# Performance work log

Measured on AMD Instinct MI355X. Metric: run time of the kernel, lower is better.

## Reference

```python
import jax, jax.numpy as jnp
import numpy as np

N = 50000
DEG = 16
E = N * DEG
IN_F, HID, OUT_F = 512, 128, 64
SLOPE = 0.2


def setup_inputs() -> dict:
    key = jax.random.key(0)
    ks = jax.random.split(key, 10)
    row_ptr = jnp.arange(N + 1, dtype=jnp.int64) * DEG          # uniform-degree CSR
    col_idx = jax.random.randint(ks[0], (E,), 0, N, dtype=jnp.int64)
    x = jax.random.normal(ks[1], (N, IN_F), dtype=jnp.float32)
    s1 = 1.0 / np.sqrt(IN_F)
    s2 = 1.0 / np.sqrt(HID)
    return {
        "row_ptr": row_ptr,
        "col_idx": col_idx,
        "input_feature": x,
        "W1": jax.random.normal(ks[2], (IN_F, HID), dtype=jnp.float32) * s1,
        "attn_l1": jax.random.normal(ks[3], (HID,), dtype=jnp.float32) * s2,
        "attn_r1": jax.random.normal(ks[4], (HID,), dtype=jnp.float32) * s2,
        "bias1": jnp.zeros((HID,), dtype=jnp.float32),
        "W2": jax.random.normal(ks[5], (HID, OUT_F), dtype=jnp.float32) * s2,
        "attn_l2": jax.random.normal(ks[6], (OUT_F,), dtype=jnp.float32) * 0.125,
        "attn_r2": jax.random.normal(ks[7], (OUT_F,), dtype=jnp.float32) * 0.125,
        "bias2": jnp.zeros((OUT_F,), dtype=jnp.float32),
    }


def gat_layer(row_ptr, col_idx, x, W, attn_l, attn_r, bias):
    n = row_ptr.shape[0] - 1
    e = col_idx.shape[0]
    h = x @ W                                   # [N, F] dense GEMM
    el = h @ attn_l                             # [N] dst attention term
    er = h @ attn_r                             # [N] src attention term
    # edge -> destination row via CSR row_ptr
    dst = jnp.searchsorted(row_ptr, jnp.arange(e, dtype=row_ptr.dtype), side="right") - 1
    src = col_idx
    score = jax.nn.leaky_relu(el[dst] + er[src], negative_slope=SLOPE)  # [E]
    # neighborhood softmax over edges sharing a destination
    smax = jax.ops.segment_max(score, dst, num_segments=n)
    ex = jnp.exp(score - smax[dst])
    ssum = jax.ops.segment_sum(ex, dst, num_segments=n)
    alpha = ex / ssum[dst]                      # [E]
    # weighted gather-scatter aggregation
    out = jax.ops.segment_sum(alpha[:, None] * h[src], dst, num_segments=n)
    return out + bias


def reference(row_ptr, col_idx, input_feature, W1, attn_l1, attn_r1, bias1,
              W2, attn_l2, attn_r2, bias2):
    x = gat_layer(row_ptr, col_idx, input_feature, W1, attn_l1, attn_r1, bias1)
    x = gat_layer(row_ptr, col_idx, x, W2, attn_l2, attn_r2, bias2)
    return x
```

## Files before the change

kernel.cpp:

```cpp
#include <hip/hip_runtime.h>
#include <hip/hip_bf16.h>

#define Nn 50000
#define DEG 16
#define IN_F 512
#define HID 128
#define OUT_F 64
#define SLOPE 0.2f

typedef __attribute__((ext_vector_type(8))) short bf16x8;
typedef __attribute__((ext_vector_type(4))) float f32x4;
typedef __attribute__((ext_vector_type(4))) unsigned int u32x4;

__device__ __forceinline__ unsigned short f2bf(float f) {
    return __builtin_bit_cast(unsigned short, __float2bfloat16(f));
}
__device__ __forceinline__ float bf2f(unsigned short u) {
    return __bfloat162float(__builtin_bit_cast(__hip_bfloat16, u));
}

__global__ void __launch_bounds__(256) prep_kernel(
        const float* __restrict__ W1, const float* __restrict__ W2,
        const float* __restrict__ al1, const float* __restrict__ ar1,
        const float* __restrict__ b1, const int* __restrict__ row_ptr,
        unsigned short* __restrict__ w12t, float* __restrict__ uv,
        float* __restrict__ c2v, int* __restrict__ flag64) {
    const int tid = threadIdx.x;
    const int lane = tid & 63;
    const int w = tid >> 6;
    const int k = blockIdx.x * 4 + w;
    if (blockIdx.x == 0 && tid == 0) {
        *flag64 = (row_ptr[1] == DEG) ? 0 : 1;
    }
    const float* w1row = W1 + (size_t)k * HID;

    float acc = 0.f;
    #pragma unroll 8
    for (int j = 0; j < HID; ++j)
        acc += w1row[j] * W2[j * OUT_F + lane];
    w12t[(size_t)lane * IN_F + k] = f2bf(acc);

    float pu = w1row[lane] * al1[lane] + w1row[lane + 64] * al1[lane + 64];
    float pv = w1row[lane] * ar1[lane] + w1row[lane + 64] * ar1[lane + 64];
    #pragma unroll
    for (int m = 1; m < 64; m <<= 1) {
        pu += __shfl_xor(pu, m);
        pv += __shfl_xor(pv, m);
    }
    if (lane == 0) { uv[k] = pu; uv[IN_F + k] = pv; }

    if (blockIdx.x == 0 && w == 0) {
        float cacc = 0.f;
        #pragma unroll 8
        for (int j = 0; j < HID; ++j) cacc += b1[j] * W2[j * OUT_F + lane];
        c2v[lane] = cacc;
    }
}

template<int K>
__global__ void __launch_bounds__(256, 6) gemm1_splitk(
        const float* __restrict__ Af, const unsigned short* __restrict__ w12t,
        const float* __restrict__ uv,
        unsigned short* __restrict__ G, float* __restrict__ el,
        float* __restrict__ er, int M) {
    constexpr int KW = K / 4;
    constexpr int RS = 20;
    __shared__ float red[4][64][RS];
    __shared__ float redl[4][16];
    __shared__ float redr[4][16];

    const int tid  = threadIdx.x;
    const int lane = tid & 63;
    const int w    = tid >> 6;
    const int ln   = lane & 15, q = lane >> 4;
    const int mb   = blockIdx.x * 16;

    const float* a0p = Af + (size_t)(mb + ln) * K + w * KW + q * 8;
    const float* up  = uv + w * KW + q * 8;
    const float* vp  = uv + K + w * KW + q * 8;

    f32x4 acc[4] = {};
    float sl = 0.f, sr = 0.f;

    f32x4 cur0 = *(const f32x4*)(a0p);
    f32x4 cur1 = *(const f32x4*)(a0p + 4);
    #pragma unroll
    for (int ks = 0; ks < 4; ++ks) {
        f32x4 nxt0, nxt1;
        if (ks < 3) {
            nxt0 = *(const f32x4*)(a0p + (ks + 1) * 32);
            nxt1 = *(const f32x4*)(a0p + (ks + 1) * 32 + 4);
        }
        f32x4 u0 = *(const f32x4*)(up + ks * 32);
        f32x4 u1 = *(const f32x4*)(up + ks * 32 + 4);
        f32x4 v0 = *(const f32x4*)(vp + ks * 32);
        f32x4 v1 = *(const f32x4*)(vp + ks * 32 + 4);
        bf16x8 af;
        #pragma unroll
        for (int jj = 0; jj < 4; ++jj) {
            af[jj]     = (short)f2bf(cur0[jj]);
            af[jj + 4] = (short)f2bf(cur1[jj]);
            sl += cur0[jj] * u0[jj] + cur1[jj] * u1[jj];
            sr += cur0[jj] * v0[jj] + cur1[jj] * v1[jj];
        }
        #pragma unroll
        for (int nt = 0; nt < 4; ++nt) {
            bf16x8 bfr = *(const bf16x8*)
                &w12t[(size_t)(nt * 16 + ln) * K + w * KW + ks * 32 + q * 8];
            acc[nt] = __builtin_amdgcn_mfma_f32_16x16x32_bf16(af, bfr, acc[nt], 0, 0, 0);
        }
        if (ks < 3) { cur0 = nxt0; cur1 = nxt1; }
    }

    #pragma unroll
    for (int nt = 0; nt < 4; ++nt)
        *(f32x4*)&red[w][nt * 16 + ln][q * 4] = acc[nt];

    sl += __shfl_xor(sl, 16); sl += __shfl_xor(sl, 32);
    sr += __shfl_xor(sr, 16); sr += __shfl_xor(sr, 32);
    if (q == 0) { redl[w][ln] = sl; redr[w][ln] = sr; }
    __syncthreads();

    const int c  = tid & 63;
    const int r0 = (tid >> 6) * 4;
    f32x4 s = *(const f32x4*)&red[0][c][r0];
    #pragma unroll
    for (int ww = 1; ww < 4; ++ww) {
        f32x4 p = *(const f32x4*)&red[ww][c][r0];
        s += p;
    }
    #pragma unroll
    for (int j = 0; j < 4; ++j)
        G[(size_t)(mb + r0 + j) * OUT_F + c] = f2bf(s[j]);

    if (tid < 16) {
        el[mb + tid] = redl[0][tid] + redl[1][tid] + redl[2][tid] + redl[3][tid];
        er[mb + tid] = redr[0][tid] + redr[1][tid] + redr[2][tid] + redr[3][tid];
    }
}

template<int MODE>
__global__ void __launch_bounds__(256) agg_k(
        const int* __restrict__ col, const int* __restrict__ flag64,
        const float* __restrict__ el, const float* __restrict__ er,
        const unsigned short* __restrict__ Hs, const float* __restrict__ addv,
        const float* __restrict__ alv, const float* __restrict__ arv,
        unsigned short* __restrict__ Ho, float* __restrict__ elo,
        float* __restrict__ ero, float* __restrict__ Fo) {
    const int tid  = threadIdx.x;
    const int lane = tid & 63;
    const int w    = tid >> 6;
    const int ln   = lane & 15, q = lane >> 4;
    const int g16  = w * 4 + q;
    const int nA   = blockIdx.x * 32 + g16 * 2;
    const int nB   = nA + 1;
    const int nAc  = nA < Nn ? nA : Nn - 1;
    const int nBc  = nB < Nn ? nB : Nn - 1;
    const int use64 = *flag64;

    int eA = nAc * DEG + ln, eB = nBc * DEG + ln;
    int srcA = use64 ? (int)((const long long*)col)[eA] : col[eA];
    int srcB = use64 ? (int)((const long long*)col)[eB] : col[eB];
    float scA = el[nAc] + er[srcA];
    float scB = el[nBc] + er[srcB];
    scA = scA >= 0.f ? scA : SLOPE * scA;
    scB = scB >= 0.f ? scB : SLOPE * scB;
    float mxA = scA, mxB = scB;
    #pragma unroll
    for (int m = 1; m < 16; m <<= 1) {
        mxA = fmaxf(mxA, __shfl_xor(mxA, m, 16));
        mxB = fmaxf(mxB, __shfl_xor(mxB, m, 16));
    }
    float exA = __expf(scA - mxA), exB = __expf(scB - mxB);
    float smA = exA, smB = exB;
    #pragma unroll
    for (int m = 1; m < 16; m <<= 1) {
        smA += __shfl_xor(smA, m, 16);
        smB += __shfl_xor(smB, m, 16);
    }
    float alA = exA / smA, alB = exB / smB;

    const int half = ln >> 3, cc = ln & 7;
    float aA[8] = {}, aB[8] = {};
    #pragma unroll
    for (int jj = 0; jj < DEG; jj += 2) {
        int   sjA = __shfl(srcA, jj + half, 16);
        float ajA = __shfl(alA,  jj + half, 16);
        int   sjB = __shfl(srcB, jj + half, 16);
        float ajB = __shfl(alB,  jj + half, 16);
        bf16x8 hA = *(const bf16x8*)&Hs[(size_t)sjA * OUT_F + cc * 8];
        bf16x8 hB = *(const bf16x8*)&Hs[(size_t)sjB * OUT_F + cc * 8];
        #pragma unroll
        for (int c = 0; c < 8; ++c) {
            aA[c] += ajA * bf2f((unsigned short)hA[c]);
            aB[c] += ajB * bf2f((unsigned short)hB[c]);
        }
    }
    #pragma unroll
    for (int c = 0; c < 8; ++c) {
        aA[c] += __shfl_xor(aA[c], 8, 16);
        aB[c] += __shfl_xor(aB[c], 8, 16);
        float ad = addv[cc * 8 + c];
        aA[c] += ad;
        aB[c] += ad;
    }

    if (MODE == 0) {
        float plA = 0.f, prA = 0.f, plB = 0.f, prB = 0.f;
        #pragma unroll
        for (int c = 0; c < 8; ++c) {
            float av = alv[cc * 8 + c], bv = arv[cc * 8 + c];
            plA += aA[c] * av;  prA += aA[c] * bv;
            plB += aB[c] * av;  prB += aB[c] * bv;
        }
        #pragma unroll
        for (int m = 1; m < 8; m <<= 1) {
            plA += __shfl_xor(plA, m, 16);  prA += __shfl_xor(prA, m, 16);
            plB += __shfl_xor(plB, m, 16);  prB += __shfl_xor(prB, m, 16);
        }
        if (ln == 0) {
            if (nA < Nn) { elo[nA] = plA; ero[nA] = prA; }
            if (nB < Nn) { elo[nB] = plB; ero[nB] = prB; }
        }
        if (half == 0) {
            unsigned int pkA[4], pkB[4];
            #pragma unroll
            for (int c = 0; c < 4; ++c) {
                pkA[c] = (unsigned int)f2bf(aA[2 * c]) |
                         ((unsigned int)f2bf(aA[2 * c + 1]) << 16);
                pkB[c] = (unsigned int)f2bf(aB[2 * c]) |
                         ((unsigned int)f2bf(aB[2 * c + 1]) << 16);
            }
            if (nA < Nn) *(u32x4*)&Ho[(size_t)nA * OUT_F + cc * 8] = *(u32x4*)pkA;
            if (nB < Nn) *(u32x4*)&Ho[(size_t)nB * OUT_F + cc * 8] = *(u32x4*)pkB;
        }
    } else {
        if (half == 0) {
            f32x4 oA0, oA1, oB0, oB1;
            #pragma unroll
            for (int c = 0; c < 4; ++c) {
                oA0[c] = aA[c]; oA1[c] = aA[c + 4];
                oB0[c] = aB[c]; oB1[c] = aB[c + 4];
            }
            if (nA < Nn) {
                *(f32x4*)&Fo[(size_t)nA * OUT_F + cc * 8]     = oA0;
                *(f32x4*)&Fo[(size_t)nA * OUT_F + cc * 8 + 4] = oA1;
            }
            if (nB < Nn) {
                *(f32x4*)&Fo[(size_t)nB * OUT_F + cc * 8]     = oB0;
                *(f32x4*)&Fo[(size_t)nB * OUT_F + cc * 8 + 4] = oB1;
            }
        }
    }
}

extern "C" void kernel_launch(void* const* d_in, const int* in_sizes, int n_in,
                              void* d_out, int out_size, void* d_ws, size_t ws_size,
                              hipStream_t stream) {
    const int*   row_ptr = (const int*)d_in[0];
    const int*   col_idx = (const int*)d_in[1];
    const float* x   = (const float*)d_in[2];
    const float* W1  = (const float*)d_in[3];
    const float* al1 = (const float*)d_in[4];
    const float* ar1 = (const float*)d_in[5];
    const float* b1  = (const float*)d_in[6];
    const float* W2  = (const float*)d_in[7];
    const float* al2 = (const float*)d_in[8];
    const float* ar2 = (const float*)d_in[9];
    const float* b2  = (const float*)d_in[10];
    float* out = (float*)d_out;

    float* ws = (float*)d_ws;
    unsigned short* g   = (unsigned short*)ws;
    unsigned short* h2b = (unsigned short*)(ws + 1600000);
    float* el1 = ws + 3200000;
    float* er1 = ws + 3250000;
    float* el2 = ws + 3300000;
    float* er2 = ws + 3350000;
    unsigned short* w12t = (unsigned short*)(ws + 3400000);
    float* uv  = ws + 3420000;
    float* c2v = ws + 3421024;
    int* flag64 = (int*)(ws + 3421100);

    prep_kernel<<<128, 256, 0, stream>>>(
        W1, W2, al1, ar1, b1, row_ptr, w12t, uv, c2v, flag64);

    gemm1_splitk<IN_F><<<Nn / 16, 256, 0, stream>>>(
        x, w12t, uv, g, el1, er1, Nn);

    agg_k<0><<<(Nn + 31) / 32, 256, 0, stream>>>(
        col_idx, flag64, el1, er1, g, c2v, al2, ar2, h2b, el2, er2, nullptr);

    agg_k<1><<<(Nn + 31) / 32, 256, 0, stream>>>(
        col_idx, flag64, el2, er2, h2b, b2, nullptr, nullptr,
        nullptr, nullptr, nullptr, out);
}
```

Measured before the change: 235.3 us.

## Replace split-K GEMM with 64-row tiled GEMM using async global-to-LDS loads

The first GEMM moves from a 16-row split-K layout, which needed a cross-wave LDS reduction, to 64-row tiles. Each wave now owns 16 rows over the full K, stepping through 128-wide chunks staged in LDS with global_load_lds async copies. The fused W1·W2 weight is stored pre-chunked with an XOR swizzle so its LDS reads avoid bank conflicts, and each block reuses it across 64 rows instead of 16. The cost is 48KB of LDS per block, which limits occupancy, and loads are not double-buffered, so each chunk waits at a barrier with no overlap.

Result: faster. 223.3 us (-5.1%).

```diff
diff --git a/kernel.cpp b/kernel.cpp
--- a/kernel.cpp
+++ b/kernel.cpp
@@ -18,12 +18,17 @@
 __device__ __forceinline__ float bf2f(unsigned short u) {
     return __bfloat162float(__builtin_bit_cast(__hip_bfloat16, u));
 }
+__device__ __forceinline__ void async_copy16(const void* g, void* l) {
+    __builtin_amdgcn_global_load_lds(
+        (const __attribute__((address_space(1))) unsigned int*)g,
+        (__attribute__((address_space(3))) unsigned int*)l, 16, 0, 0);
+}
 
 __global__ void __launch_bounds__(256) prep_kernel(
         const float* __restrict__ W1, const float* __restrict__ W2,
         const float* __restrict__ al1, const float* __restrict__ ar1,
         const float* __restrict__ b1, const int* __restrict__ row_ptr,
-        unsigned short* __restrict__ w12t, float* __restrict__ uv,
+        unsigned short* __restrict__ w12c, float* __restrict__ uv,
         float* __restrict__ c2v, int* __restrict__ flag64) {
     const int tid = threadIdx.x;
     const int lane = tid & 63;
@@ -38,7 +43,12 @@
     #pragma unroll 8
     for (int j = 0; j < HID; ++j)
         acc += w1row[j] * W2[j * OUT_F + lane];
-    w12t[(size_t)lane * IN_F + k] = f2bf(acc);
+    {
+        int ch = k >> 7, kin = k & 127;
+        int bsrc = kin >> 3, j = kin & 7;
+        int bdst = bsrc ^ (lane & 7);
+        w12c[ch * 8192 + lane * 128 + bdst * 8 + j] = f2bf(acc);
+    }
 
     float pu = w1row[lane] * al1[lane] + w1row[lane + 64] * al1[lane + 64];
     float pv = w1row[lane] * ar1[lane] + w1row[lane + 64] * ar1[lane + 64];
@@ -58,84 +68,85 @@
 }
 
 template<int K>
-__global__ void __launch_bounds__(256, 6) gemm1_splitk(
-        const float* __restrict__ Af, const unsigned short* __restrict__ w12t,
+__global__ void __launch_bounds__(256) gemm1_tiled(
+        const float* __restrict__ Af, const unsigned short* __restrict__ w12c,
         const float* __restrict__ uv,
         unsigned short* __restrict__ G, float* __restrict__ el,
         float* __restrict__ er, int M) {
-    constexpr int KW = K / 4;
-    constexpr int RS = 20;
-    __shared__ float red[4][64][RS];
-    __shared__ float redl[4][16];
-    __shared__ float redr[4][16];
+    constexpr int NCH = K / 128;
+    __shared__ float As[64 * 128];
+    __shared__ unsigned short Bs[64 * 128];
 
     const int tid  = threadIdx.x;
     const int lane = tid & 63;
     const int w    = tid >> 6;
     const int ln   = lane & 15, q = lane >> 4;
-    const int mb   = blockIdx.x * 16;
-
-    const float* a0p = Af + (size_t)(mb + ln) * K + w * KW + q * 8;
-    const float* up  = uv + w * KW + q * 8;
-    const float* vp  = uv + K + w * KW + q * 8;
+    const int r2   = lane >> 5, b = lane & 31;
+    const int mb   = blockIdx.x * 64;
 
     f32x4 acc[4] = {};
     float sl = 0.f, sr = 0.f;
 
-    f32x4 cur0 = *(const f32x4*)(a0p);
-    f32x4 cur1 = *(const f32x4*)(a0p + 4);
-    #pragma unroll
-    for (int ks = 0; ks < 4; ++ks) {
-        f32x4 nxt0, nxt1;
-        if (ks < 3) {
-            nxt0 = *(const f32x4*)(a0p + (ks + 1) * 32);
-            nxt1 = *(const f32x4*)(a0p + (ks + 1) * 32 + 4);
-        }
-        f32x4 u0 = *(const f32x4*)(up + ks * 32);
-        f32x4 u1 = *(const f32x4*)(up + ks * 32 + 4);
-        f32x4 v0 = *(const f32x4*)(vp + ks * 32);
-        f32x4 v1 = *(const f32x4*)(vp + ks * 32 + 4);
-        bf16x8 af;
-        #pragma unroll
-        for (int jj = 0; jj < 4; ++jj) {
-            af[jj]     = (short)f2bf(cur0[jj]);
-            af[jj + 4] = (short)f2bf(cur1[jj]);
-            sl += cur0[jj] * u0[jj] + cur1[jj] * u1[jj];
-            sr += cur0[jj] * v0[jj] + cur1[jj] * v1[jj];
-        }
-        #pragma unroll
-        for (int nt = 0; nt < 4; ++nt) {
-            bf16x8 bfr = *(const bf16x8*)
-                &w12t[(size_t)(nt * 16 + ln) * K + w * KW + ks * 32 + q * 8];
-            acc[nt] = __builtin_amdgcn_mfma_f32_16x16x32_bf16(af, bfr, acc[nt], 0, 0, 0);
-        }
-        if (ks < 3) { cur0 = nxt0; cur1 = nxt1; }
-    }
-
-    #pragma unroll
-    for (int nt = 0; nt < 4; ++nt)
-        *(f32x4*)&red[w][nt * 16 + ln][q * 4] = acc[nt];
+    for (int ch = 0; ch < NCH; ++ch) {
+        const char* gb = (const char*)w12c + ch * 16384;
+        #pragma unroll
+        for (int i = 0; i < 4; ++i) {
+            int slot = w * 4 + i;
+            async_copy16(gb + slot * 1024 + lane * 16, (char*)Bs + slot * 1024);
+        }
+        #pragma unroll
+        for (int i = 0; i < 8; ++i) {
+            int rl = w * 16 + i * 2 + r2;
+            int rg = mb + rl; if (rg > M - 1) rg = M - 1;
+            int c  = rl & 7;
+            const float* src = Af + (size_t)rg * K + ch * 128 + ((b ^ c) << 2);
+            async_copy16(src, (char*)As + (size_t)(w * 16 + i * 2) * 512);
+        }
+        __syncthreads();
+
+        const float* up = uv + ch * 128;
+        const float* vp = uv + K + ch * 128;
+        const int c = ln & 7;
+        #pragma unroll
+        for (int ks = 0; ks < 4; ++ks) {
+            const int b0 = ks * 8 + q * 2;
+            f32x4 a0 = *(const f32x4*)&As[(w * 16 + ln) * 128 + ((b0 ^ c) << 2)];
+            f32x4 a1 = *(const f32x4*)&As[(w * 16 + ln) * 128 + (((b0 + 1) ^ c) << 2)];
+            f32x4 u0 = *(const f32x4*)(up + ks * 32 + q * 8);
+            f32x4 u1 = *(const f32x4*)(up + ks * 32 + q * 8 + 4);
+            f32x4 v0 = *(const f32x4*)(vp + ks * 32 + q * 8);
+            f32x4 v1 = *(const f32x4*)(vp + ks * 32 + q * 8 + 4);
+            bf16x8 af;
+            #pragma unroll
+            for (int jj = 0; jj < 4; ++jj) {
+                af[jj]     = (short)f2bf(a0[jj]);
+                af[jj + 4] = (short)f2bf(a1[jj]);
+                sl += a0[jj] * u0[jj] + a1[jj] * u1[jj];
+                sr += a0[jj] * v0[jj] + a1[jj] * v1[jj];
+            }
+            #pragma unroll
+            for (int nt = 0; nt < 4; ++nt) {
+                const int bb = ks * 4 + q;
+                bf16x8 bfr = *(const bf16x8*)&Bs[(nt * 16 + ln) * 128 + ((bb ^ c) << 3)];
+                acc[nt] = __builtin_amdgcn_mfma_f32_16x16x32_bf16(af, bfr, acc[nt], 0, 0, 0);
+            }
+        }
+        __syncthreads();
+    }
 
     sl += __shfl_xor(sl, 16); sl += __shfl_xor(sl, 32);
     sr += __shfl_xor(sr, 16); sr += __shfl_xor(sr, 32);
-    if (q == 0) { redl[w][ln] = sl; redr[w][ln] = sr; }
-    __syncthreads();
-
-    const int c  = tid & 63;
-    const int r0 = (tid >> 6) * 4;
-    f32x4 s = *(const f32x4*)&red[0][c][r0];
-    #pragma unroll
-    for (int ww = 1; ww < 4; ++ww) {
-        f32x4 p = *(const f32x4*)&red[ww][c][r0];
-        s += p;
-    }
-    #pragma unroll
-    for (int j = 0; j < 4; ++j)
-        G[(size_t)(mb + r0 + j) * OUT_F + c] = f2bf(s[j]);
-
-    if (tid < 16) {
-        el[mb + tid] = redl[0][tid] + redl[1][tid] + redl[2][tid] + redl[3][tid];
-        er[mb + tid] = redr[0][tid] + redr[1][tid] + redr[2][tid] + redr[3][tid];
+    const int rowe = mb + w * 16 + ln;
+    if (q == 0 && rowe < M) { el[rowe] = sl; er[rowe] = sr; }
+
+    #pragma unroll
+    for (int r = 0; r < 4; ++r) {
+        int grow = mb + w * 16 + q * 4 + r;
+        if (grow < M) {
+            #pragma unroll
+            for (int nt = 0; nt < 4; ++nt)
+                G[(size_t)grow * OUT_F + nt * 16 + ln] = f2bf(acc[nt][r]);
+        }
     }
 }
 
@@ -277,16 +288,16 @@
     float* er1 = ws + 3250000;
     float* el2 = ws + 3300000;
     float* er2 = ws + 3350000;
-    unsigned short* w12t = (unsigned short*)(ws + 3400000);
+    unsigned short* w12c = (unsigned short*)(ws + 3400000);
     float* uv  = ws + 3420000;
     float* c2v = ws + 3421024;
     int* flag64 = (int*)(ws + 3421100);
 
     prep_kernel<<<128, 256, 0, stream>>>(
-        W1, W2, al1, ar1, b1, row_ptr, w12t, uv, c2v, flag64);
-
-    gemm1_splitk<IN_F><<<Nn / 16, 256, 0, stream>>>(
-        x, w12t, uv, g, el1, er1, Nn);
+        W1, W2, al1, ar1, b1, row_ptr, w12c, uv, c2v, flag64);
+
+    gemm1_tiled<IN_F><<<(Nn + 63) / 64, 256, 0, stream>>>(
+        x, w12c, uv, g, el1, er1, Nn);
 
     agg_k<0><<<(Nn + 31) / 32, 256, 0, stream>>>(
         col_idx, flag64, el1, er1, g, c2v, al2, ar2, h2b, el2, er2, nullptr);
```

## Stage GEMM A-tile via async global-to-LDS copies and batch gather loads

Applied to the files above, without the earlier changes.

The first-layer GEMM now loads each block's 16x512 fp32 input tile into LDS with coalesced global_load_lds copies using an XOR swizzle. Each wave then reads its K-slice from shared memory instead of issuing strided per-lane global loads, and the LDS buffer is reused afterwards for the split-K reduction. The aggregation kernel issues all eight neighbor-row gathers up front before accumulating, so more memory requests are in flight at once. In exchange, the GEMM uses 32KB of LDS per block, drops the occupancy hint, and needs extra barriers, and the aggregation kernel holds more registers.

After: 242.6 us. +3.1%, slower.

```diff
diff --git a/kernel.cpp b/kernel.cpp
--- a/kernel.cpp
+++ b/kernel.cpp
@@ -17,6 +17,11 @@
 }
 __device__ __forceinline__ float bf2f(unsigned short u) {
     return __bfloat162float(__builtin_bit_cast(__hip_bfloat16, u));
+}
+__device__ __forceinline__ void async_copy16(const void* g, void* l) {
+    __builtin_amdgcn_global_load_lds(
+        (const __attribute__((address_space(1))) unsigned int*)g,
+        (__attribute__((address_space(3))) unsigned int*)l, 16, 0, 0);
 }
 
 __global__ void __launch_bounds__(256) prep_kernel(
@@ -58,16 +63,17 @@
 }
 
 template<int K>
-__global__ void __launch_bounds__(256, 6) gemm1_splitk(
+__global__ void __launch_bounds__(256) gemm1_lin(
         const float* __restrict__ Af, const unsigned short* __restrict__ w12t,
         const float* __restrict__ uv,
         unsigned short* __restrict__ G, float* __restrict__ el,
         float* __restrict__ er, int M) {
-    constexpr int KW = K / 4;
-    constexpr int RS = 20;
-    __shared__ float red[4][64][RS];
+    __shared__ char ldsbuf[16 * 512 * 4];
     __shared__ float redl[4][16];
     __shared__ float redr[4][16];
+    float* As = (float*)ldsbuf;
+    typedef float redt[64][20];
+    redt* red = (redt*)ldsbuf;
 
     const int tid  = threadIdx.x;
     const int lane = tid & 63;
@@ -75,42 +81,45 @@
     const int ln   = lane & 15, q = lane >> 4;
     const int mb   = blockIdx.x * 16;
 
-    const float* a0p = Af + (size_t)(mb + ln) * K + w * KW + q * 8;
-    const float* up  = uv + w * KW + q * 8;
-    const float* vp  = uv + K + w * KW + q * 8;
+    #pragma unroll
+    for (int i = 0; i < 8; ++i) {
+        int j   = w * 8 + i;
+        int row = j >> 1;
+        int b   = (j & 1) * 64 + lane;
+        int c   = row & 7;
+        const float* src = Af + (size_t)(mb + row) * K + ((b ^ c) << 2);
+        async_copy16(src, ldsbuf + j * 1024);
+    }
+    __syncthreads();
 
     f32x4 acc[4] = {};
     float sl = 0.f, sr = 0.f;
-
-    f32x4 cur0 = *(const f32x4*)(a0p);
-    f32x4 cur1 = *(const f32x4*)(a0p + 4);
+    const int c7 = ln & 7;
     #pragma unroll
     for (int ks = 0; ks < 4; ++ks) {
-        f32x4 nxt0, nxt1;
-        if (ks < 3) {
-            nxt0 = *(const f32x4*)(a0p + (ks + 1) * 32);
-            nxt1 = *(const f32x4*)(a0p + (ks + 1) * 32 + 4);
-        }
-        f32x4 u0 = *(const f32x4*)(up + ks * 32);
-        f32x4 u1 = *(const f32x4*)(up + ks * 32 + 4);
-        f32x4 v0 = *(const f32x4*)(vp + ks * 32);
-        f32x4 v1 = *(const f32x4*)(vp + ks * 32 + 4);
+        const int B0 = w * 32 + ks * 8 + q * 2;
+        f32x4 a0 = *(const f32x4*)&As[ln * 512 + ((B0 ^ c7) << 2)];
+        f32x4 a1 = *(const f32x4*)&As[ln * 512 + (((B0 + 1) ^ c7) << 2)];
+        const int ko = w * 128 + ks * 32 + q * 8;
+        f32x4 u0 = *(const f32x4*)(uv + ko);
+        f32x4 u1 = *(const f32x4*)(uv + ko + 4);
+        f32x4 v0 = *(const f32x4*)(uv + K + ko);
+        f32x4 v1 = *(const f32x4*)(uv + K + ko + 4);
         bf16x8 af;
         #pragma unroll
         for (int jj = 0; jj < 4; ++jj) {
-            af[jj]     = (short)f2bf(cur0[jj]);
-            af[jj + 4] = (short)f2bf(cur1[jj]);
-            sl += cur0[jj] * u0[jj] + cur1[jj] * u1[jj];
-            sr += cur0[jj] * v0[jj] + cur1[jj] * v1[jj];
+            af[jj]     = (short)f2bf(a0[jj]);
+            af[jj + 4] = (short)f2bf(a1[jj]);
+            sl += a0[jj] * u0[jj] + a1[jj] * u1[jj];
+            sr += a0[jj] * v0[jj] + a1[jj] * v1[jj];
         }
         #pragma unroll
         for (int nt = 0; nt < 4; ++nt) {
-            bf16x8 bfr = *(const bf16x8*)
-                &w12t[(size_t)(nt * 16 + ln) * K + w * KW + ks * 32 + q * 8];
+            bf16x8 bfr = *(const bf16x8*)&w12t[(size_t)(nt * 16 + ln) * K + ko];
             acc[nt] = __builtin_amdgcn_mfma_f32_16x16x32_bf16(af, bfr, acc[nt], 0, 0, 0);
         }
-        if (ks < 3) { cur0 = nxt0; cur1 = nxt1; }
-    }
+    }
+    __syncthreads();
 
     #pragma unroll
     for (int nt = 0; nt < 4; ++nt)
@@ -121,17 +130,17 @@
     if (q == 0) { redl[w][ln] = sl; redr[w][ln] = sr; }
     __syncthreads();
 
-    const int c  = tid & 63;
+    const int cc = tid & 63;
     const int r0 = (tid >> 6) * 4;
-    f32x4 s = *(const f32x4*)&red[0][c][r0];
+    f32x4 s = *(const f32x4*)&red[0][cc][r0];
     #pragma unroll
     for (int ww = 1; ww < 4; ++ww) {
-        f32x4 p = *(const f32x4*)&red[ww][c][r0];
+        f32x4 p = *(const f32x4*)&red[ww][cc][r0];
         s += p;
     }
     #pragma unroll
     for (int j = 0; j < 4; ++j)
-        G[(size_t)(mb + r0 + j) * OUT_F + c] = f2bf(s[j]);
+        G[(size_t)(mb + r0 + j) * OUT_F + cc] = f2bf(s[j]);
 
     if (tid < 16) {
         el[mb + tid] = redl[0][tid] + redl[1][tid] + redl[2][tid] + redl[3][tid];
@@ -181,19 +190,23 @@
     float alA = exA / smA, alB = exB / smB;
 
     const int half = ln >> 3, cc = ln & 7;
+    bf16x8 hA[8], hB[8];
+    #pragma unroll
+    for (int p = 0; p < 8; ++p) {
+        int sjA = __shfl(srcA, p * 2 + half, 16);
+        int sjB = __shfl(srcB, p * 2 + half, 16);
+        hA[p] = *(const bf16x8*)&Hs[(size_t)sjA * OUT_F + cc * 8];
+        hB[p] = *(const bf16x8*)&Hs[(size_t)sjB * OUT_F + cc * 8];
+    }
     float aA[8] = {}, aB[8] = {};
     #pragma unroll
-    for (int jj = 0; jj < DEG; jj += 2) {
-        int   sjA = __shfl(srcA, jj + half, 16);
-        float ajA = __shfl(alA,  jj + half, 16);
-        int   sjB = __shfl(srcB, jj + half, 16);
-        float ajB = __shfl(alB,  jj + half, 16);
-        bf16x8 hA = *(const bf16x8*)&Hs[(size_t)sjA * OUT_F + cc * 8];
-        bf16x8 hB = *(const bf16x8*)&Hs[(size_t)sjB * OUT_F + cc * 8];
+    for (int p = 0; p < 8; ++p) {
+        float wA = __shfl(alA, p * 2 + half, 16);
+        float wB = __shfl(alB, p * 2 + half, 16);
         #pragma unroll
         for (int c = 0; c < 8; ++c) {
-            aA[c] += ajA * bf2f((unsigned short)hA[c]);
-            aB[c] += ajB * bf2f((unsigned short)hB[c]);
+            aA[c] += wA * bf2f((unsigned short)hA[p][c]);
+            aB[c] += wB * bf2f((unsigned short)hB[p][c]);
         }
     }
     #pragma unroll
@@ -285,7 +298,7 @@
     prep_kernel<<<128, 256, 0, stream>>>(
         W1, W2, al1, ar1, b1, row_ptr, w12t, uv, c2v, flag64);
 
-    gemm1_splitk<IN_F><<<Nn / 16, 256, 0, stream>>>(
+    gemm1_lin<IN_F><<<Nn / 16, 256, 0, stream>>>(
         x, w12t, uv, g, el1, er1, Nn);
 
     agg_k<0><<<(Nn + 31) / 32, 256, 0, stream>>>(
```
